# Kernel tuning notes

Hardware: AMD Instinct MI355X
Metric: run time of the kernel (lower is better)

Reference implementation:

```python
import jax, jax.numpy as jnp
import numpy as np

B, N, C, H, D = 1, 4096, 256, 8, 64  # batch, seq, channels, heads, head_dim


def setup_inputs() -> dict:
    key = jax.random.key(0)
    ks = jax.random.split(key, 11)
    s = 0.02
    return {
        "q_x": jax.random.normal(ks[0], (B, N, C), jnp.float32),
        "k_x": jax.random.normal(ks[1], (B, N, C), jnp.float32),
        "v_x": jax.random.normal(ks[2], (B, N, C), jnp.float32),
        "bias": jax.random.normal(ks[3], (B, 1, N, N), jnp.float32),
        "wq": jax.random.normal(ks[4], (H * D, C), jnp.float32) * s,
        "wk": jax.random.normal(ks[5], (H * D, C), jnp.float32) * s,
        "wv": jax.random.normal(ks[6], (H * D, C), jnp.float32) * s,
        "wg": jax.random.normal(ks[7], (H * D, C), jnp.float32) * s,
        "bg": jnp.ones((H * D,), jnp.float32),  # gating bias init = 1
        "wo": jax.random.normal(ks[8], (C, H * D), jnp.float32) * s,
        "bo": jnp.zeros((C,), jnp.float32),
        "q_chunk_size": 256,
        "kv_chunk_size": 1024,
    }


def reference(q_x, k_x, v_x, bias, wq, wk, wv, wg, bg, wo, bo,
              q_chunk_size, kv_chunk_size):
    # The chunked Rabe-Staats loop computes exact softmax attention; the
    # chunk sizes are memory knobs only, so the reference computes the
    # mathematically identical full attention.
    q = (q_x @ wq.T).reshape(*q_x.shape[:-1], H, D) / jnp.sqrt(jnp.asarray(D, q_x.dtype))
    k = (k_x @ wk.T).reshape(*k_x.shape[:-1], H, D)
    v = (v_x @ wv.T).reshape(*v_x.shape[:-1], H, D)
    logits = jnp.einsum("bqhd,bkhd->bhqk", q, k) + bias  # [B,H,Q,K]
    p = jax.nn.softmax(logits, axis=-1)
    o = jnp.einsum("bkhd,bhqk->bqhd", v, p)  # [B,Q,H,D]
    g = jax.nn.sigmoid(q_x @ wg.T + bg).reshape(*q_x.shape[:-1], H, D)
    o = o * g
    o = o.reshape(*o.shape[:-2], H * D)
    return o @ wo.T + bo
```

## Files before the change

### kernel.cpp

```cpp
#include <hip/hip_runtime.h>
#include <stdint.h>

#define NN 4096
#define CC 256
#define HD 512
#define DD 64
#define KSPLIT 3

typedef __attribute__((ext_vector_type(8))) short short8;
typedef __attribute__((ext_vector_type(4))) float floatx4;

__device__ __forceinline__ unsigned short f2bf(float x) {
    union { float f; unsigned int u; } v; v.f = x;
    unsigned int u = v.u + 0x7fffu + ((v.u >> 16) & 1u);
    return (unsigned short)(u >> 16);
}
__device__ __forceinline__ float bf2f(unsigned short s) {
    union { unsigned int u; float f; } v; v.u = ((unsigned int)s) << 16;
    return v.f;
}

#if defined(__has_builtin) && __has_builtin(__builtin_amdgcn_cvt_pk_bf16_f32)
typedef __attribute__((ext_vector_type(2))) __bf16 bf16x2_t;
__device__ __forceinline__ unsigned int pack2bf(float a, float b) {
    union { bf16x2_t v; unsigned int u; } x;
    x.v = __builtin_amdgcn_cvt_pk_bf16_f32(a, b);
    return x.u;
}
#else
__device__ __forceinline__ unsigned int pack2bf(float a, float b) {
    return ((unsigned int)f2bf(b) << 16) | (unsigned int)f2bf(a);
}
#endif

#define GLOAD_LDS(gp, lp) __builtin_amdgcn_global_load_lds(                    \
    (__attribute__((address_space(1))) void*)(gp),                             \
    (__attribute__((address_space(3))) void*)(lp), 16, 0, 0)

__global__ __launch_bounds__(256) void prep_kernel(
    const float* __restrict__ qx, const float* __restrict__ kx,
    const float* __restrict__ vx,
    const float* __restrict__ wq, const float* __restrict__ wk,
    const float* __restrict__ wv, const float* __restrict__ wg,
    const float* __restrict__ wo,
    unsigned short* __restrict__ qxb, unsigned short* __restrict__ kxb,
    unsigned short* __restrict__ vxb, unsigned short* __restrict__ Wb,
    unsigned short* __restrict__ wob)
{
    const int z = blockIdx.y;
    const float* src; unsigned short* dst; int n; float s = 1.0f;
    switch (z) {
        case 0: src = qx; dst = qxb; n = NN * CC; break;
        case 1: src = kx; dst = kxb; n = NN * CC; break;
        case 2: src = vx; dst = vxb; n = NN * CC; break;
        case 3: src = wq; dst = Wb;               n = HD * CC; s = 0.125f; break;
        case 4: src = wk; dst = Wb + 1 * HD * CC; n = HD * CC; break;
        case 5: src = wv; dst = Wb + 2 * HD * CC; n = HD * CC; break;
        case 6: src = wg; dst = Wb + 3 * HD * CC; n = HD * CC; break;
        default: src = wo; dst = wob;             n = CC * HD; break;
    }
    int i = (blockIdx.x * 256 + threadIdx.x) * 4;
    if (i < n) {
        float4 v = *(const float4*)&src[i];
        ushort4 p;
        p.x = f2bf(v.x * s); p.y = f2bf(v.y * s);
        p.z = f2bf(v.z * s); p.w = f2bf(v.w * s);
        *(ushort4*)&dst[i] = p;
    }
}

__global__ __launch_bounds__(256, 8) void proj_kernel(
    const unsigned short* __restrict__ qxb, const unsigned short* __restrict__ kxb,
    const unsigned short* __restrict__ vxb, const unsigned short* __restrict__ Wb,
    const float* __restrict__ bg,
    unsigned short* __restrict__ Qb, unsigned short* __restrict__ Kb,
    unsigned short* __restrict__ VbT, unsigned short* __restrict__ Gb)
{
    const int m0 = blockIdx.x * 64;
    const int nb = blockIdx.y;
    const int mode = nb >> 3;
    const int subn = nb & 7;
    const int n0 = mode * HD + subn * 64;
    const unsigned short* X = (mode == 1) ? kxb : (mode == 2) ? vxb : qxb;

    const int tid = threadIdx.x;
    const int wid = tid >> 6;
    const int lane = tid & 63;
    const int quad = lane >> 4;
    const int ln = lane & 15;
    const int lnx = ln & 7;

    __shared__ __align__(16) unsigned short smem[2 * 64 * 64];
    unsigned short* Xs = smem;
    unsigned short* Ws = smem + 64 * 64;

    floatx4 acc[4] = {};

    for (int k0 = 0; k0 < CC; k0 += 64) {
        #pragma unroll
        for (int t = 0; t < 2; t++) {
            int row = wid * 16 + t * 8 + (lane >> 3);
            int c = (lane & 7) ^ (lane >> 3);
            GLOAD_LDS(&X[(size_t)(m0 + row) * CC + k0 + c * 8],
                      &Xs[(wid * 16 + t * 8) * 64]);
            GLOAD_LDS(&Wb[(size_t)(n0 + row) * CC + k0 + c * 8],
                      &Ws[(wid * 16 + t * 8) * 64]);
        }
        __syncthreads();

        #pragma unroll
        for (int ks = 0; ks < 64; ks += 32) {
            const int cb = ks >> 3;
            short8 a = *(const short8*)&Xs[(wid * 16 + ln) * 64 +
                                           (((quad ^ cb) ^ lnx) * 8)];
            #pragma unroll
            for (int n = 0; n < 4; n++) {
                short8 b = *(const short8*)&Ws[(n * 16 + ln) * 64 +
                                               (((quad ^ cb) ^ lnx) * 8)];
                acc[n] = __builtin_amdgcn_mfma_f32_16x16x32_bf16(a, b, acc[n], 0, 0, 0);
            }
        }
        __syncthreads();
    }

    if (mode != 2) {
        unsigned short* Out = (mode == 0) ? Qb : (mode == 1) ? Kb : Gb;
        #pragma unroll
        for (int n = 0; n < 4; n++) {
            int col = subn * 64 + n * 16 + ln;
            float bgv = (mode == 3) ? bg[col] : 0.0f;
            #pragma unroll
            for (int r = 0; r < 4; r++) {
                int row = m0 + wid * 16 + quad * 4 + r;
                float v = acc[n][r];
                if (mode == 3) v = 1.0f / (1.0f + __expf(-(v + bgv)));
                Out[(size_t)row * HD + col] = f2bf(v);
            }
        }
    } else {
        #pragma unroll
        for (int n = 0; n < 4; n++) {
            int cl = n * 16 + ln;
            #pragma unroll
            for (int r = 0; r < 4; r++) {
                int rl = wid * 16 + quad * 4 + r;
                smem[cl * 72 + rl] = f2bf(acc[n][r]);
            }
        }
        __syncthreads();
        #pragma unroll
        for (int it = 0; it < 2; it++) {
            int idx = it * 256 + tid;
            int c = idx >> 3, ch = idx & 7;
            short8 vv = *(const short8*)&smem[c * 72 + ch * 8];
            *(short8*)&VbT[(size_t)(subn * 64 + c) * NN + m0 + ch * 8] = vv;
        }
    }
}

__global__ __launch_bounds__(256, 6) void attn_kernel(
    const unsigned short* __restrict__ Qb, const unsigned short* __restrict__ Kb,
    const unsigned short* __restrict__ VbT,
    const float* __restrict__ bias,
    unsigned short* __restrict__ Opart, float* __restrict__ Lpart)
{
    const int h = blockIdx.y;
    const int q0 = blockIdx.x * 64;
    const int sp = blockIdx.z;
    const int tbeg = (sp * 64) / KSPLIT;
    const int tend = ((sp + 1) * 64) / KSPLIT;
    const int tid = threadIdx.x;
    const int wid = tid >> 6;
    const int lane = tid & 63;
    const int quad = lane >> 4;
    const int ln = lane & 15;
    const int lnx = ln & 7;

    __shared__ __align__(16) unsigned short Ks[64 * 64];
    __shared__ __align__(16) unsigned short Vs[64 * 64];
    __shared__ __align__(16) unsigned short Ps[64 * 72];

    const int qrow = q0 + wid * 16 + ln;
    short8 qa0 = *(const short8*)&Qb[(size_t)qrow * HD + h * DD + quad * 8];
    short8 qa1 = *(const short8*)&Qb[(size_t)qrow * HD + h * DD + 32 + quad * 8];

    floatx4 O[4] = {};
    float lsum[4] = {0.0f, 0.0f, 0.0f, 0.0f};

    for (int kt = tbeg; kt < tend; kt++) {
        const int k0 = kt * 64;
        #pragma unroll
        for (int t = 0; t < 2; t++) {
            int row = wid * 16 + t * 8 + (lane >> 3);
            int c = (lane & 7) ^ (lane >> 3);
            GLOAD_LDS(&Kb[(size_t)(k0 + row) * HD + h * DD + c * 8],
                      &Ks[(wid * 16 + t * 8) * 64]);
            GLOAD_LDS(&VbT[(size_t)(h * DD + row) * NN + k0 + c * 8],
                      &Vs[(wid * 16 + t * 8) * 64]);
        }

        float bv[4][4];
        #pragma unroll
        for (int r = 0; r < 4; r++) {
            const float* brow = &bias[(size_t)(q0 + wid * 16 + quad * 4 + r) * NN + k0];
            #pragma unroll
            for (int n = 0; n < 4; n++) bv[r][n] = brow[n * 16 + ln];
        }
        __syncthreads();

        floatx4 S[4];
        #pragma unroll
        for (int n = 0; n < 4; n++)
            S[n] = (floatx4){bv[0][n], bv[1][n], bv[2][n], bv[3][n]};
        #pragma unroll
        for (int n = 0; n < 4; n++) {
            short8 b0 = *(const short8*)&Ks[(n * 16 + ln) * 64 + ((quad ^ lnx) * 8)];
            S[n] = __builtin_amdgcn_mfma_f32_16x16x32_bf16(qa0, b0, S[n], 0, 0, 0);
            short8 b1 = *(const short8*)&Ks[(n * 16 + ln) * 64 + (((quad ^ 4) ^ lnx) * 8)];
            S[n] = __builtin_amdgcn_mfma_f32_16x16x32_bf16(qa1, b1, S[n], 0, 0, 0);
        }

        #pragma unroll
        for (int r = 0; r < 4; r++) {
            int prow = (wid * 16 + quad * 4 + r) * 72;
            #pragma unroll
            for (int n = 0; n < 4; n += 2) {
                float p0 = __expf(S[n][r]);
                float p1 = __expf(S[n + 1][r]);
                lsum[r] += p0 + p1;
                unsigned int pk = pack2bf(p0, p1);
                Ps[prow + n * 16 + ln] = (unsigned short)(pk & 0xffffu);
                Ps[prow + (n + 1) * 16 + ln] = (unsigned short)(pk >> 16);
            }
        }

        #pragma unroll
        for (int ks = 0; ks < 64; ks += 32) {
            const int cb = ks >> 3;
            short8 a = *(const short8*)&Ps[(wid * 16 + ln) * 72 + ks + quad * 8];
            #pragma unroll
            for (int nd = 0; nd < 4; nd++) {
                short8 b = *(const short8*)&Vs[(nd * 16 + ln) * 64 +
                                               (((quad ^ cb) ^ lnx) * 8)];
                O[nd] = __builtin_amdgcn_mfma_f32_16x16x32_bf16(a, b, O[nd], 0, 0, 0);
            }
        }
        __syncthreads();
    }

    #pragma unroll
    for (int r = 0; r < 4; r++) {
        #pragma unroll
        for (int off = 1; off < 16; off <<= 1)
            lsum[r] += __shfl_xor(lsum[r], off);
        int grow = q0 + wid * 16 + quad * 4 + r;
        size_t base = ((size_t)(sp * 8 + h) * NN + grow) * 64;
        #pragma unroll
        for (int nd = 0; nd < 4; nd++)
            Opart[base + nd * 16 + ln] = f2bf(O[nd][r]);
        if (ln == 0)
            Lpart[(size_t)(sp * 8 + h) * NN + grow] = lsum[r];
    }
}

__global__ __launch_bounds__(256) void combine_kernel(
    const unsigned short* __restrict__ Opart, const float* __restrict__ Lpart,
    const unsigned short* __restrict__ Gb, unsigned short* __restrict__ OGb)
{
    const int tid = threadIdx.x;
    const int flat = blockIdx.x * 32 + (tid >> 3);
    const int h = flat >> 12;
    const int q = flat & (NN - 1);
    const int d0 = (tid & 7) * 8;

    float l = 0.0f;
    float ov[8] = {};
    #pragma unroll
    for (int sp = 0; sp < KSPLIT; sp++) {
        size_t idx = (size_t)(sp * 8 + h) * NN + q;
        l += Lpart[idx];
        short8 o8 = *(const short8*)&Opart[idx * 64 + d0];
        #pragma unroll
        for (int j = 0; j < 8; j++) ov[j] += bf2f((unsigned short)o8[j]);
    }
    float inv = 1.0f / l;
    short8 g8 = *(const short8*)&Gb[(size_t)q * HD + h * DD + d0];
    union { unsigned int u[4]; short8 s; } pk;
    #pragma unroll
    for (int j = 0; j < 4; j++)
        pk.u[j] = pack2bf(ov[2 * j] * inv * bf2f((unsigned short)g8[2 * j]),
                          ov[2 * j + 1] * inv * bf2f((unsigned short)g8[2 * j + 1]));
    *(short8*)&OGb[(size_t)q * HD + h * DD + d0] = pk.s;
}

__global__ __launch_bounds__(256, 2) void outproj_kernel(
    const unsigned short* __restrict__ OGb, const unsigned short* __restrict__ wob,
    const float* __restrict__ bo, float* __restrict__ out)
{
    const int m0 = blockIdx.x * 32;
    const int n0 = blockIdx.y * 64;
    const int tid = threadIdx.x;
    const int wid = tid >> 6;
    const int wr = wid >> 1, wc = wid & 1;
    const int lane = tid & 63;
    const int quad = lane >> 4;
    const int ln = lane & 15;
    const int lnx = ln & 7;

    __shared__ __align__(16) unsigned short Xs[2][32 * 64];
    __shared__ __align__(16) unsigned short Ws[2][64 * 64];

    floatx4 acc[2] = {};

    auto STAGE = [&](int k0, int bf) {
        int c = (lane & 7) ^ (lane >> 3);
        int xrow = wid * 8 + (lane >> 3);
        GLOAD_LDS(&OGb[(size_t)(m0 + xrow) * HD + k0 + c * 8],
                  &Xs[bf][(wid * 8) * 64]);
        #pragma unroll
        for (int t = 0; t < 2; t++) {
            int wrow = wid * 16 + t * 8 + (lane >> 3);
            GLOAD_LDS(&wob[(size_t)(n0 + wrow) * HD + k0 + c * 8],
                      &Ws[bf][(wid * 16 + t * 8) * 64]);
        }
    };

    STAGE(0, 0);
    __syncthreads();

    for (int it = 0; it < 8; it++) {
        const int bf = it & 1;
        if (it + 1 < 8) STAGE((it + 1) * 64, bf ^ 1);

        #pragma unroll
        for (int ks = 0; ks < 64; ks += 32) {
            const int cb = ks >> 3;
            short8 a = *(const short8*)&Xs[bf][(wr * 16 + ln) * 64 +
                                              (((quad ^ cb) ^ lnx) * 8)];
            #pragma unroll
            for (int j = 0; j < 2; j++) {
                short8 b = *(const short8*)&Ws[bf][(wc * 32 + j * 16 + ln) * 64 +
                                                   (((quad ^ cb) ^ lnx) * 8)];
                acc[j] = __builtin_amdgcn_mfma_f32_16x16x32_bf16(a, b, acc[j], 0, 0, 0);
            }
        }
        __syncthreads();
    }

    #pragma unroll
    for (int j = 0; j < 2; j++) {
        int col = n0 + wc * 32 + j * 16 + ln;
        float bov = bo[col];
        #pragma unroll
        for (int r = 0; r < 4; r++) {
            int row = m0 + wr * 16 + quad * 4 + r;
            out[(size_t)row * CC + col] = acc[j][r] + bov;
        }
    }
}

extern "C" void kernel_launch(void* const* d_in, const int* in_sizes, int n_in,
                              void* d_out, int out_size, void* d_ws, size_t ws_size,
                              hipStream_t stream) {
    const float* qx   = (const float*)d_in[0];
    const float* kx   = (const float*)d_in[1];
    const float* vx   = (const float*)d_in[2];
    const float* bias = (const float*)d_in[3];
    const float* wq   = (const float*)d_in[4];
    const float* wk   = (const float*)d_in[5];
    const float* wv   = (const float*)d_in[6];
    const float* wg   = (const float*)d_in[7];
    const float* bg   = (const float*)d_in[8];
    const float* wo   = (const float*)d_in[9];
    const float* bo   = (const float*)d_in[10];
    float* out = (float*)d_out;

    char* ws = (char*)d_ws;
    const size_t MB = (size_t)1 << 20;
    unsigned short* wob   = (unsigned short*)(ws);
    float*          Lpart = (float*)(ws + MB / 4);
    unsigned short* Qb    = (unsigned short*)(ws + 1 * MB);
    unsigned short* Kb    = (unsigned short*)(ws + 5 * MB);
    unsigned short* VbT   = (unsigned short*)(ws + 9 * MB);
    unsigned short* Gb    = (unsigned short*)(ws + 13 * MB);
    unsigned short* OGb   = (unsigned short*)(ws + 17 * MB);
    unsigned short* qxb   = (unsigned short*)(ws + 21 * MB);
    unsigned short* kxb   = (unsigned short*)(ws + 23 * MB);
    unsigned short* vxb   = (unsigned short*)(ws + 25 * MB);
    unsigned short* Wb    = (unsigned short*)(ws + 27 * MB);
    unsigned short* Opart = (unsigned short*)(ws + 21 * MB);

    prep_kernel<<<dim3(NN * CC / (256 * 4), 8), 256, 0, stream>>>(
        qx, kx, vx, wq, wk, wv, wg, wo, qxb, kxb, vxb, Wb, wob);
    proj_kernel<<<dim3(64, 32), 256, 0, stream>>>(
        qxb, kxb, vxb, Wb, bg, Qb, Kb, VbT, Gb);
    attn_kernel<<<dim3(64, 8, KSPLIT), 256, 0, stream>>>(
        Qb, Kb, VbT, bias, Opart, Lpart);
    combine_kernel<<<dim3(NN * 8 / 32), 256, 0, stream>>>(
        Opart, Lpart, Gb, OGb);
    outproj_kernel<<<dim3(128, 4), 256, 0, stream>>>(
        OGb, wob, bo, out);
}
```

Before: 210.3 us.

## Compute transposed QK^T so P stays in registers, assembled via lane shuffles

The QK^T MFMA operands are swapped so each lane holds a column of S (one query row, four key positions). The probabilities are then packed into the A-operand layout for the PV MFMA using cross-lane shuffles instead of a round trip through LDS. Bias is loaded as contiguous float4 per lane, and the row-sum reduction shrinks to two shuffles. This removes the Ps LDS writes and reads and a strided bias gather, at the cost of extra shuffle and select instructions. The shared array is sized larger than K and V need, but only K and V are used.

```diff
diff --git a/kernel.cpp b/kernel.cpp
--- a/kernel.cpp
+++ b/kernel.cpp
@@ -176,16 +176,33 @@
     const int ln = lane & 15;
     const int lnx = ln & 7;
 
-    __shared__ __align__(16) unsigned short Ks[64 * 64];
-    __shared__ __align__(16) unsigned short Vs[64 * 64];
-    __shared__ __align__(16) unsigned short Ps[64 * 72];
+    __shared__ __align__(16) unsigned short smem[12320];
+    unsigned short* Ks = smem;
+    unsigned short* Vs = smem + 4096;
 
     const int qrow = q0 + wid * 16 + ln;
     short8 qa0 = *(const short8*)&Qb[(size_t)qrow * HD + h * DD + quad * 8];
     short8 qa1 = *(const short8*)&Qb[(size_t)qrow * HD + h * DD + 32 + quad * 8];
 
     floatx4 O[4] = {};
-    float lsum[4] = {0.0f, 0.0f, 0.0f, 0.0f};
+    float lsum = 0.0f;
+
+    const float* brow = &bias[(size_t)qrow * NN + quad * 4];
+
+    auto ASSEMBLE = [&](const unsigned int* pA, const unsigned int* pB) -> short8 {
+        unsigned int s16_0 = __shfl_xor((quad < 2)  ? pA[0] : pB[0], 16);
+        unsigned int s16_1 = __shfl_xor((quad < 2)  ? pA[1] : pB[1], 16);
+        unsigned int s32_0 = __shfl_xor((quad == 3) ? pA[0] : pB[0], 32);
+        unsigned int s32_1 = __shfl_xor((quad == 3) ? pA[1] : pB[1], 32);
+        unsigned int s48_0 = __shfl_xor((quad == 2) ? pA[0] : pB[0], 48);
+        unsigned int s48_1 = __shfl_xor((quad == 2) ? pA[1] : pB[1], 48);
+        union { unsigned int u[4]; short8 s; } w;
+        w.u[0] = (quad == 0) ? pA[0] : (quad == 1) ? s48_0 : (quad == 2) ? s32_0 : s16_0;
+        w.u[1] = (quad == 0) ? pA[1] : (quad == 1) ? s48_1 : (quad == 2) ? s32_1 : s16_1;
+        w.u[2] = (quad == 0) ? s16_0 : (quad == 1) ? s32_0 : (quad == 2) ? s48_0 : pB[0];
+        w.u[3] = (quad == 0) ? s16_1 : (quad == 1) ? s32_1 : (quad == 2) ? s48_1 : pB[1];
+        return w.s;
+    };
 
     for (int kt = tbeg; kt < tend; kt++) {
         const int k0 = kt * 64;
@@ -199,68 +216,64 @@
                       &Vs[(wid * 16 + t * 8) * 64]);
         }
 
-        float bv[4][4];
-        #pragma unroll
-        for (int r = 0; r < 4; r++) {
-            const float* brow = &bias[(size_t)(q0 + wid * 16 + quad * 4 + r) * NN + k0];
-            #pragma unroll
-            for (int n = 0; n < 4; n++) bv[r][n] = brow[n * 16 + ln];
-        }
-        __syncthreads();
-
         floatx4 S[4];
         #pragma unroll
-        for (int n = 0; n < 4; n++)
-            S[n] = (floatx4){bv[0][n], bv[1][n], bv[2][n], bv[3][n]};
+        for (int n = 0; n < 4; n++) {
+            float4 b4 = *(const float4*)&brow[k0 + n * 16];
+            S[n] = (floatx4){b4.x, b4.y, b4.z, b4.w};
+        }
+        __syncthreads();
+
         #pragma unroll
         for (int n = 0; n < 4; n++) {
             short8 b0 = *(const short8*)&Ks[(n * 16 + ln) * 64 + ((quad ^ lnx) * 8)];
-            S[n] = __builtin_amdgcn_mfma_f32_16x16x32_bf16(qa0, b0, S[n], 0, 0, 0);
+            S[n] = __builtin_amdgcn_mfma_f32_16x16x32_bf16(b0, qa0, S[n], 0, 0, 0);
             short8 b1 = *(const short8*)&Ks[(n * 16 + ln) * 64 + (((quad ^ 4) ^ lnx) * 8)];
-            S[n] = __builtin_amdgcn_mfma_f32_16x16x32_bf16(qa1, b1, S[n], 0, 0, 0);
-        }
-
-        #pragma unroll
-        for (int r = 0; r < 4; r++) {
-            int prow = (wid * 16 + quad * 4 + r) * 72;
-            #pragma unroll
-            for (int n = 0; n < 4; n += 2) {
-                float p0 = __expf(S[n][r]);
-                float p1 = __expf(S[n + 1][r]);
-                lsum[r] += p0 + p1;
-                unsigned int pk = pack2bf(p0, p1);
-                Ps[prow + n * 16 + ln] = (unsigned short)(pk & 0xffffu);
-                Ps[prow + (n + 1) * 16 + ln] = (unsigned short)(pk >> 16);
-            }
-        }
+            S[n] = __builtin_amdgcn_mfma_f32_16x16x32_bf16(b1, qa1, S[n], 0, 0, 0);
+        }
+
+        unsigned int pk[4][2];
+        #pragma unroll
+        for (int n = 0; n < 4; n++) {
+            float p0 = __expf(S[n][0]);
+            float p1 = __expf(S[n][1]);
+            float p2 = __expf(S[n][2]);
+            float p3 = __expf(S[n][3]);
+            lsum += (p0 + p1) + (p2 + p3);
+            pk[n][0] = pack2bf(p0, p1);
+            pk[n][1] = pack2bf(p2, p3);
+        }
+
+        short8 pa0 = ASSEMBLE(pk[0], pk[1]);
+        short8 pa1 = ASSEMBLE(pk[2], pk[3]);
 
         #pragma unroll
         for (int ks = 0; ks < 64; ks += 32) {
             const int cb = ks >> 3;
-            short8 a = *(const short8*)&Ps[(wid * 16 + ln) * 72 + ks + quad * 8];
+            short8 a = (ks == 0) ? pa0 : pa1;
             #pragma unroll
             for (int nd = 0; nd < 4; nd++) {
-                short8 b = *(const short8*)&Vs[(nd * 16 + ln) * 64 +
-                                               (((quad ^ cb) ^ lnx) * 8)];
-                O[nd] = __builtin_amdgcn_mfma_f32_16x16x32_bf16(a, b, O[nd], 0, 0, 0);
+                short8 vb = *(const short8*)&Vs[(nd * 16 + ln) * 64 +
+                                                (((quad ^ cb) ^ lnx) * 8)];
+                O[nd] = __builtin_amdgcn_mfma_f32_16x16x32_bf16(a, vb, O[nd], 0, 0, 0);
             }
         }
         __syncthreads();
     }
+
+    float lt = lsum + __shfl_xor(lsum, 16);
+    lt += __shfl_xor(lt, 32);
 
     #pragma unroll
     for (int r = 0; r < 4; r++) {
-        #pragma unroll
-        for (int off = 1; off < 16; off <<= 1)
-            lsum[r] += __shfl_xor(lsum[r], off);
         int grow = q0 + wid * 16 + quad * 4 + r;
         size_t base = ((size_t)(sp * 8 + h) * NN + grow) * 64;
         #pragma unroll
         for (int nd = 0; nd < 4; nd++)
             Opart[base + nd * 16 + ln] = f2bf(O[nd][r]);
-        if (ln == 0)
-            Lpart[(size_t)(sp * 8 + h) * NN + grow] = lsum[r];
-    }
+    }
+    if (lane < 16)
+        Lpart[(size_t)(sp * 8 + h) * NN + qrow] = lt;
 }
 
 __global__ __launch_bounds__(256) void combine_kernel(
```

New measurement: 248.1 us. 1.18x slower.
